# Kernel optimization log

Measured on AMD Instinct MI355X. Metric: run time of the kernel, lower is better.

The kernel has to match this reference:

```python
import jax, jax.numpy as jnp
import numpy as np

OT_REG = 0.1      # entropic regularization (ot_reg)
OT_TAU = 0.5      # marginal relaxation (ot_tau / reg_m)
N_ITERS = 100     # fixed Sinkhorn iterations (POT uses numItermax=1000 w/ stopThr=1e-6; 100 is converged here)


def setup_inputs() -> dict:
    key = jax.random.key(0)
    k1, k2 = jax.random.split(key)
    x = jax.random.normal(k1, (1, 4096, 1024), dtype=jnp.float32)
    y = jax.random.normal(k2, (1, 2048, 1024), dtype=jnp.float32)
    return {"x": x, "y": y}


def _sq_cdist(a, b):
    # torch.cdist(a, b) ** 2  ==  squared Euclidean pairwise distances, [N, M]
    d = (jnp.sum(a * a, axis=1)[:, None]
         + jnp.sum(b * b, axis=1)[None, :]
         - 2.0 * (a @ b.T))
    return jnp.maximum(d, 0.0)


def reference(x, y):
    # forward: squeeze leading batch dim, shift features to be >= 0 per row
    x = jnp.squeeze(x, axis=0)                      # [N, D]
    y = jnp.squeeze(y, axis=0)                      # [M, D]
    x = x - jnp.min(x, axis=-1, keepdims=True)
    y = y - jnp.min(y, axis=-1, keepdims=True)

    C = _sq_cdist(x, y)                              # [N, M] cost map (differentiable)
    n, m = C.shape

    # POT sinkhorn_knopp_unbalanced on detached, max-normalized cost
    Mn = jax.lax.stop_gradient(C)
    Mn = Mn / jnp.max(Mn)
    K = jnp.exp(-Mn / OT_REG)                        # Gibbs kernel
    a = jnp.full((n,), 1.0 / n, dtype=C.dtype)       # uniform source marginal
    b = jnp.full((m,), 1.0 / m, dtype=C.dtype)       # uniform target marginal
    fi = OT_TAU / (OT_TAU + OT_REG)

    def body(i, uv):
        u, v = uv
        u = (a / (K @ v)) ** fi
        v = (b / (K.T @ u)) ** fi
        return (u, v)

    u0 = jnp.full((n,), 1.0 / n, dtype=C.dtype)
    v0 = jnp.full((m,), 1.0 / m, dtype=C.dtype)
    u, v = jax.lax.fori_loop(0, N_ITERS, body, (u0, v0))

    flow = u[:, None] * K * v[None, :]               # [N, M] transport plan
    flow = jax.lax.stop_gradient(flow)               # plan is detached in original (numpy roundtrip)
    dist = jnp.sum(C * flow)                         # OT distance w/ grad through C only

    return flow.T[None], dist                        # pi.T.unsqueeze(0): [1, M, N]
```

## Files before the change

kernel.cpp:

```cpp
#include <hip/hip_runtime.h>


#define NROWS 4096
#define MCOLS 2048
#define NITER 100
#define NBLK  256
#define SPEC_TICKS 85ull

using short8  = __attribute__((ext_vector_type(8))) short;
using floatx4 = __attribute__((ext_vector_type(4))) float;

__device__ __forceinline__ float bf2f(unsigned short u) {
  return __uint_as_float(((unsigned)u) << 16);
}
__device__ __forceinline__ unsigned short f2bf(float f) {
  unsigned u = __float_as_uint(f);
  u += 0x7fffu + ((u >> 16) & 1u);
  return (unsigned short)(u >> 16);
}
__device__ __forceinline__ float powfi(float x, float fi) {
  return __expf(fi * __logf(x));
}
__device__ __forceinline__ unsigned packsp(float v, unsigned parity) {
  return __float_as_uint(v) | (parity << 31);
}
__device__ __forceinline__ unsigned aload(const unsigned* p) {
  return __hip_atomic_load(p, __ATOMIC_RELAXED, __HIP_MEMORY_SCOPE_AGENT);
}
__device__ __forceinline__ void astore(unsigned* p, unsigned v) {
  __hip_atomic_store(p, v, __ATOMIC_RELAXED, __HIP_MEMORY_SCOPE_AGENT);
}
__device__ __forceinline__ void gload_lds16(const unsigned short* gsrc, unsigned short* ldst) {
  __builtin_amdgcn_global_load_lds(
      (const __attribute__((address_space(1))) void*)gsrc,
      (__attribute__((address_space(3))) void*)ldst, 16, 0, 0);
}

__global__ __launch_bounds__(256) void prep_kernel(
    const float* __restrict__ x, const float* __restrict__ y,
    unsigned short* __restrict__ xb, unsigned short* __restrict__ yb,
    float* __restrict__ nx, float* __restrict__ ny,
    unsigned* __restrict__ maxCbits, float* __restrict__ out,
    unsigned* __restrict__ uglob, unsigned* __restrict__ vglob,
    unsigned* __restrict__ ublkflag, unsigned* __restrict__ vblkflag,
    unsigned* __restrict__ uroot, unsigned* __restrict__ vroot) {
  const int row = blockIdx.x;
  const int tid = threadIdx.x;

  if (row == 0) {
    if (tid == 0) { *maxCbits = 0u; out[8388608] = 0.0f; }
    #pragma unroll
    for (int k = 0; k < 16; ++k) uglob[tid + (k << 8)] = 0u;
    #pragma unroll
    for (int k = 0; k < 8; ++k) vglob[tid + (k << 8)] = 0u;
    ublkflag[tid] = 0u;
    vblkflag[tid] = 0u;
    if (tid < 32) { uroot[tid * 32] = 0u; vroot[tid * 32] = 0u; }
  }

  const float* src; unsigned short* dst; float* nd;
  if (row < NROWS) { src = x + (size_t)row * 1024; dst = xb + (size_t)row * 1024; nd = nx + row; }
  else { const int r = row - NROWS; src = y + (size_t)r * 1024; dst = yb + (size_t)r * 1024; nd = ny + r; }

  float4 v = ((const float4*)src)[tid];
  float mn = fminf(fminf(v.x, v.y), fminf(v.z, v.w));
  #pragma unroll
  for (int m = 1; m < 64; m <<= 1) mn = fminf(mn, __shfl_xor(mn, m));
  __shared__ float wred[4];
  const int w = tid >> 6, l = tid & 63;
  if (l == 0) wred[w] = mn;
  __syncthreads();
  mn = fminf(fminf(wred[0], wred[1]), fminf(wred[2], wred[3]));
  __syncthreads();

  const unsigned short b0 = f2bf(v.x - mn), b1 = f2bf(v.y - mn);
  const unsigned short b2 = f2bf(v.z - mn), b3 = f2bf(v.w - mn);
  ushort4 ub; ub.x = b0; ub.y = b1; ub.z = b2; ub.w = b3;
  ((ushort4*)dst)[tid] = ub;
  const float f0 = bf2f(b0), f1 = bf2f(b1), f2 = bf2f(b2), f3 = bf2f(b3);
  float acc = f0 * f0 + f1 * f1 + f2 * f2 + f3 * f3;
  #pragma unroll
  for (int m = 1; m < 64; m <<= 1) acc += __shfl_xor(acc, m);
  if (l == 0) wred[w] = acc;
  __syncthreads();
  if (tid == 0) *nd = wred[0] + wred[1] + wred[2] + wred[3];
}

__global__ __launch_bounds__(256) void cost_gemm_kernel(
    const unsigned short* __restrict__ xb, const unsigned short* __restrict__ yb,
    const float* __restrict__ nx, const float* __restrict__ ny,
    float* __restrict__ C, unsigned* __restrict__ maxCbits) {
  __shared__ __align__(16) unsigned short As[128 * 64];
  __shared__ __align__(16) unsigned short Bs[128 * 64];

  const int tid = threadIdx.x;
  const int w = tid >> 6, l = tid & 63;
  const int wr = w >> 1, wc = w & 1;
  const int i0 = blockIdx.y * 128;
  const int j0 = blockIdx.x * 128;
  const int m16 = l & 15, q = l >> 4;

  const int st_row = tid >> 3;
  const int st_s   = tid & 7;

  floatx4 acc[4][4];
  #pragma unroll
  for (int a = 0; a < 4; ++a)
    #pragma unroll
    for (int b = 0; b < 4; ++b) acc[a][b] = (floatx4){0.f, 0.f, 0.f, 0.f};

  for (int k0 = 0; k0 < 1024; k0 += 64) {
    #pragma unroll
    for (int c = 0; c < 4; ++c) {
      const int row = c * 32 + st_row;
      const int ss = st_s ^ (row & 7);
      gload_lds16(xb + (size_t)(i0 + row) * 1024 + k0 + ss * 8,
                  &As[c * 2048 + tid * 8]);
    }
    #pragma unroll
    for (int c = 0; c < 4; ++c) {
      const int row = c * 32 + st_row;
      const int ss = st_s ^ (row & 7);
      gload_lds16(yb + (size_t)(j0 + row) * 1024 + k0 + ss * 8,
                  &Bs[c * 2048 + tid * 8]);
    }
    __syncthreads();

    #pragma unroll
    for (int kk = 0; kk < 2; ++kk) {
      short8 av[4], bv[4];
      #pragma unroll
      for (int t = 0; t < 4; ++t) {
        const int row = wr * 64 + t * 16 + m16;
        const int slot = (kk * 4 + q) ^ (row & 7);
        av[t] = *(const short8*)&As[row * 64 + slot * 8];
      }
      #pragma unroll
      for (int t = 0; t < 4; ++t) {
        const int row = wc * 64 + t * 16 + m16;
        const int slot = (kk * 4 + q) ^ (row & 7);
        bv[t] = *(const short8*)&Bs[row * 64 + slot * 8];
      }
      #pragma unroll
      for (int ti = 0; ti < 4; ++ti)
        #pragma unroll
        for (int tj = 0; tj < 4; ++tj)
          acc[ti][tj] = __builtin_amdgcn_mfma_f32_16x16x32_bf16(av[ti], bv[tj], acc[ti][tj], 0, 0, 0);
    }
    __syncthreads();
  }

  float mx = 0.f;
  #pragma unroll
  for (int ti = 0; ti < 4; ++ti) {
    #pragma unroll
    for (int tj = 0; tj < 4; ++tj) {
      const int i = i0 + wr * 64 + ti * 16 + q * 4;
      const int j = j0 + wc * 64 + tj * 16 + m16;
      const float nyj = ny[j];
      #pragma unroll
      for (int r = 0; r < 4; ++r) {
        float c = nx[i + r] + nyj - 2.0f * acc[ti][tj][r];
        c = fmaxf(c, 0.0f);
        C[(size_t)(i + r) * 2048 + j] = c;
        mx = fmaxf(mx, c);
      }
    }
  }
  __shared__ float mred[4];
  #pragma unroll
  for (int m = 1; m < 64; m <<= 1) mx = fmaxf(mx, __shfl_xor(mx, m));
  if (l == 0) mred[w] = mx;
  __syncthreads();
  if (tid == 0) {
    const float bm = fmaxf(fmaxf(mred[0], mred[1]), fmaxf(mred[2], mred[3]));
    atomicMax(maxCbits, __float_as_uint(bm));
  }
}

__global__ __launch_bounds__(512) void sinkhorn_kernel(
    const float* __restrict__ C, const unsigned* __restrict__ maxCbits,
    unsigned* __restrict__ uglob, unsigned* __restrict__ vglob,
    unsigned* __restrict__ ublkflag, unsigned* __restrict__ vblkflag,
    unsigned* __restrict__ uroot, unsigned* __restrict__ vroot,
    float* __restrict__ out) {
  __shared__ __align__(16) unsigned short Ks[16 * 2048];
  __shared__ __align__(16) unsigned short KsT[8 * 4096];
  __shared__ __align__(16) float us[4096];
  __shared__ __align__(16) float vs[2048];
  __shared__ __align__(16) float uloc[16];
  __shared__ float dred[8];
  __shared__ unsigned needretry;

  const int tid = threadIdx.x;
  const int bid = blockIdx.x;
  const int w = tid >> 6, l = tid & 63;
  const int i0 = bid * 16;
  const int jb = bid * 8;

  const float fi = 0.8333333333333334f;
  const float av = 1.0f / 4096.0f;
  const float bv = 1.0f / 2048.0f;

  {
    if (tid == 0) needretry = 0u;
    const float sc = -1.0f / (0.1f * __uint_as_float(*maxCbits));
    for (int il = 0; il < 16; ++il) {
      const float* cp = C + (size_t)(i0 + il) * 2048 + tid * 4;
      const float4 c0 = *(const float4*)cp;
      uint2 pk;
      pk.x = (unsigned)f2bf(__expf(c0.x * sc)) | ((unsigned)f2bf(__expf(c0.y * sc)) << 16);
      pk.y = (unsigned)f2bf(__expf(c0.z * sc)) | ((unsigned)f2bf(__expf(c0.w * sc)) << 16);
      *(uint2*)&Ks[il * 2048 + tid * 4] = pk;
    }
    #pragma unroll
    for (int k = 0; k < 8; ++k) {
      const int i = tid + (k << 9);
      const float* cp = C + (size_t)i * 2048 + jb;
      const float4 c0 = *(const float4*)cp;
      const float4 c1 = *(const float4*)(cp + 4);
      KsT[0 * 4096 + i] = f2bf(__expf(c0.x * sc));
      KsT[1 * 4096 + i] = f2bf(__expf(c0.y * sc));
      KsT[2 * 4096 + i] = f2bf(__expf(c0.z * sc));
      KsT[3 * 4096 + i] = f2bf(__expf(c0.w * sc));
      KsT[4 * 4096 + i] = f2bf(__expf(c1.x * sc));
      KsT[5 * 4096 + i] = f2bf(__expf(c1.y * sc));
      KsT[6 * 4096 + i] = f2bf(__expf(c1.z * sc));
      KsT[7 * 4096 + i] = f2bf(__expf(c1.w * sc));
    }
    *(float4*)&vs[tid * 4] = make_float4(bv, bv, bv, bv);
  }
  __syncthreads();

  for (int it = 1; it <= NITER; ++it) {
    const unsigned tagit = (unsigned)it;
    const unsigned par = tagit & 1u;

    float part[2] = {0.f, 0.f};
    const int r0 = w * 2;
    #pragma unroll
    for (int c = 0; c < 4; ++c) {
      const int j0 = c * 512 + l * 8;
      const float4 va = *(const float4*)&vs[j0];
      const float4 vb = *(const float4*)&vs[j0 + 4];
      #pragma unroll
      for (int rr = 0; rr < 2; ++rr) {
        const uint4 kb = *(const uint4*)&Ks[(r0 + rr) * 2048 + j0];
        part[rr] += bf2f((unsigned short)kb.x) * va.x + bf2f((unsigned short)(kb.x >> 16)) * va.y
                 +  bf2f((unsigned short)kb.y) * va.z + bf2f((unsigned short)(kb.y >> 16)) * va.w
                 +  bf2f((unsigned short)kb.z) * vb.x + bf2f((unsigned short)(kb.z >> 16)) * vb.y
                 +  bf2f((unsigned short)kb.w) * vb.z + bf2f((unsigned short)(kb.w >> 16)) * vb.w;
      }
    }
    #pragma unroll
    for (int m = 1; m < 64; m <<= 1) {
      part[0] += __shfl_xor(part[0], m);
      part[1] += __shfl_xor(part[1], m);
    }
    if (l == 0) {
      #pragma unroll
      for (int r = 0; r < 2; ++r) {
        const float uv = powfi(av / part[r], fi);
        uloc[r0 + r] = uv;
        astore(&uglob[i0 + r0 + r], packsp(uv, par));
      }
    }
    __builtin_amdgcn_s_barrier();
    if (tid == 0) astore(&ublkflag[bid], tagit);
    const unsigned long long udl = __builtin_amdgcn_s_memrealtime() + SPEC_TICKS;

    if (bid == 0) {
      if (tid < 256)
        while ((int)(aload(&ublkflag[tid]) - tagit) < 0) __builtin_amdgcn_s_sleep(1);
      __builtin_amdgcn_s_barrier();
      if (tid < 32) astore(&uroot[tid * 32], tagit);
    }

    while (__builtin_amdgcn_s_memrealtime() < udl) __builtin_amdgcn_s_sleep(1);
    {
      unsigned pend = 0xFFu;
      unsigned gu[8];
      #pragma unroll
      for (int k = 0; k < 8; ++k)
        gu[k] = aload(&uglob[tid + (k << 9)]);
      #pragma unroll
      for (int k = 0; k < 8; ++k)
        if ((gu[k] >> 31) == par) {
          us[tid + (k << 9)] = __uint_as_float(gu[k] & 0x7FFFFFFFu);
          pend &= ~(1u << k);
        }
      if (pend) {
        #pragma unroll
        for (int k = 0; k < 8; ++k)
          if (pend & (1u << k))
            gu[k] = aload(&uglob[tid + (k << 9)]);
        #pragma unroll
        for (int k = 0; k < 8; ++k)
          if ((pend & (1u << k)) && (gu[k] >> 31) == par) {
            us[tid + (k << 9)] = __uint_as_float(gu[k] & 0x7FFFFFFFu);
            pend &= ~(1u << k);
          }
      }
      if (pend) atomicOr(&needretry, 1u);
      __syncthreads();
      if (needretry) {
        if (tid == 0)
          while ((int)(aload(&uroot[(bid & 31) * 32]) - tagit) < 0) __builtin_amdgcn_s_sleep(1);
        __syncthreads();
        while (pend) {
          #pragma unroll
          for (int k = 0; k < 8; ++k)
            if (pend & (1u << k))
              gu[k] = aload(&uglob[tid + (k << 9)]);
          #pragma unroll
          for (int k = 0; k < 8; ++k)
            if ((pend & (1u << k)) && (gu[k] >> 31) == par) {
              us[tid + (k << 9)] = __uint_as_float(gu[k] & 0x7FFFFFFFu);
              pend &= ~(1u << k);
            }
          if (pend) __builtin_amdgcn_s_sleep(1);
        }
        if (tid == 0) needretry = 0u;
        __syncthreads();
      }
    }

    {
      float t0 = 0.f;
      const int ca = w * 4096;
      #pragma unroll
      for (int c = 0; c < 8; ++c) {
        const int ic = c * 512 + l * 8;
        const float4 ua = *(const float4*)&us[ic];
        const float4 ub = *(const float4*)&us[ic + 4];
        const uint4 ka = *(const uint4*)&KsT[ca + ic];
        t0 += bf2f((unsigned short)ka.x) * ua.x + bf2f((unsigned short)(ka.x >> 16)) * ua.y
           +  bf2f((unsigned short)ka.y) * ua.z + bf2f((unsigned short)(ka.y >> 16)) * ua.w
           +  bf2f((unsigned short)ka.z) * ub.x + bf2f((unsigned short)(ka.z >> 16)) * ub.y
           +  bf2f((unsigned short)ka.w) * ub.z + bf2f((unsigned short)(ka.w >> 16)) * ub.w;
      }
      #pragma unroll
      for (int m = 1; m < 64; m <<= 1) t0 += __shfl_xor(t0, m);
      if (l == 0)
        astore(&vglob[jb + w], packsp(powfi(bv / t0, fi), par));
    }
    __builtin_amdgcn_s_barrier();
    if (tid == 0) astore(&vblkflag[bid], tagit);
    const unsigned long long vdl = __builtin_amdgcn_s_memrealtime() + SPEC_TICKS;

    if (bid == 1) {
      if (tid < 256)
        while ((int)(aload(&vblkflag[tid]) - tagit) < 0) __builtin_amdgcn_s_sleep(1);
      __builtin_amdgcn_s_barrier();
      if (tid < 32) astore(&vroot[tid * 32], tagit);
    }

    while (__builtin_amdgcn_s_memrealtime() < vdl) __builtin_amdgcn_s_sleep(1);
    {
      unsigned pend = 0xFu;
      unsigned gv[4];
      #pragma unroll
      for (int k = 0; k < 4; ++k)
        gv[k] = aload(&vglob[tid + (k << 9)]);
      #pragma unroll
      for (int k = 0; k < 4; ++k)
        if ((gv[k] >> 31) == par) {
          vs[tid + (k << 9)] = __uint_as_float(gv[k] & 0x7FFFFFFFu);
          pend &= ~(1u << k);
        }
      if (pend) {
        #pragma unroll
        for (int k = 0; k < 4; ++k)
          if (pend & (1u << k))
            gv[k] = aload(&vglob[tid + (k << 9)]);
        #pragma unroll
        for (int k = 0; k < 4; ++k)
          if ((pend & (1u << k)) && (gv[k] >> 31) == par) {
            vs[tid + (k << 9)] = __uint_as_float(gv[k] & 0x7FFFFFFFu);
            pend &= ~(1u << k);
          }
      }
      if (pend) atomicOr(&needretry, 1u);
      __syncthreads();
      if (needretry) {
        if (tid == 0)
          while ((int)(aload(&vroot[(bid & 31) * 32]) - tagit) < 0) __builtin_amdgcn_s_sleep(1);
        __syncthreads();
        while (pend) {
          #pragma unroll
          for (int k = 0; k < 4; ++k)
            if (pend & (1u << k))
              gv[k] = aload(&vglob[tid + (k << 9)]);
          #pragma unroll
          for (int k = 0; k < 4; ++k)
            if ((pend & (1u << k)) && (gv[k] >> 31) == par) {
              vs[tid + (k << 9)] = __uint_as_float(gv[k] & 0x7FFFFFFFu);
              pend &= ~(1u << k);
            }
          if (pend) __builtin_amdgcn_s_sleep(1);
        }
        if (tid == 0) needretry = 0u;
        __syncthreads();
      }
    }
  }

  float ur[16];
  *(float4*)&ur[0]  = *(const float4*)&uloc[0];
  *(float4*)&ur[4]  = *(const float4*)&uloc[4];
  *(float4*)&ur[8]  = *(const float4*)&uloc[8];
  *(float4*)&ur[12] = *(const float4*)&uloc[12];
  float distp = 0.f;
  for (int sub = 0; sub < 4; ++sub) {
    const int j = w * 256 + sub * 64 + l;
    const float vj = vs[j];
    float o[16];
    #pragma unroll
    for (int il = 0; il < 16; ++il) {
      const float kf = bf2f(Ks[il * 2048 + j]);
      const float fl = ur[il] * kf * vj;
      o[il] = fl;
      distp += C[(size_t)(i0 + il) * 2048 + j] * fl;
    }
    float* op = out + (size_t)j * 4096 + i0;
    *(float4*)(op)      = make_float4(o[0],  o[1],  o[2],  o[3]);
    *(float4*)(op + 4)  = make_float4(o[4],  o[5],  o[6],  o[7]);
    *(float4*)(op + 8)  = make_float4(o[8],  o[9],  o[10], o[11]);
    *(float4*)(op + 12) = make_float4(o[12], o[13], o[14], o[15]);
  }
  #pragma unroll
  for (int m = 1; m < 64; m <<= 1) distp += __shfl_xor(distp, m);
  if (l == 0) dred[w] = distp;
  __syncthreads();
  if (tid == 0) {
    float ds = 0.f;
    #pragma unroll
    for (int k = 0; k < 8; ++k) ds += dred[k];
    unsafeAtomicAdd(out + (size_t)8388608, ds);
  }
}

extern "C" void kernel_launch(void* const* d_in, const int* in_sizes, int n_in,
                              void* d_out, int out_size, void* d_ws, size_t ws_size,
                              hipStream_t stream) {
  (void)in_sizes; (void)n_in; (void)out_size; (void)ws_size;
  const float* x = (const float*)d_in[0];
  const float* y = (const float*)d_in[1];
  float* out = (float*)d_out;
  char* ws = (char*)d_ws;

  float*              Cmat     = (float*)(ws + 0);
  unsigned short*     xb       = (unsigned short*)(ws + 33554432);
  unsigned short*     yb       = (unsigned short*)(ws + 41943040);
  float*              nx       = (float*)(ws + 46137344);
  float*              ny       = (float*)(ws + 46153728);
  unsigned*           maxC     = (unsigned*)(ws + 46161920);
  unsigned*           uglob    = (unsigned*)(ws + 46162432);
  unsigned*           vglob    = (unsigned*)(ws + 46178816);
  unsigned*           ublkflag = (unsigned*)(ws + 46187008);
  unsigned*           vblkflag = (unsigned*)(ws + 46188032);
  unsigned*           uroot    = (unsigned*)(ws + 46189056);
  unsigned*           vroot    = (unsigned*)(ws + 46193152);

  hipLaunchKernelGGL(prep_kernel, dim3(6144), dim3(256), 0, stream, x, y, xb, yb, nx, ny,
                     maxC, out, uglob, vglob, ublkflag, vblkflag, uroot, vroot);
  hipLaunchKernelGGL(cost_gemm_kernel, dim3(16, 32), dim3(256), 0, stream, xb, yb, nx, ny, Cmat, maxC);
  hipLaunchKernelGGL(sinkhorn_kernel, dim3(NBLK), dim3(512), 0, stream,
                     Cmat, maxC, uglob, vglob, ublkflag, vblkflag, uroot, vroot, out);
}
```

Baseline: 638.5 us.

## Double Sinkhorn block size to 1024 threads, one row per wave

Launches the persistent Sinkhorn kernel with 1024 threads per block instead of 512. Each of the 16 waves now handles one u-row, and pairs of waves split each v-column dot product, combined through shared memory. The gather, setup and epilogue loops are re-indexed for the larger block. The goal is to shorten the per-iteration critical path by spreading the matvec work over more waves. The cost is an extra __syncthreads and shared reduction in the v step, plus higher register pressure under the 1024-thread launch bound.

```diff
diff --git a/kernel.cpp b/kernel.cpp
--- a/kernel.cpp
+++ b/kernel.cpp
@@ -178,7 +178,7 @@
   }
 }
 
-__global__ __launch_bounds__(512) void sinkhorn_kernel(
+__global__ __launch_bounds__(1024) void sinkhorn_kernel(
     const float* __restrict__ C, const unsigned* __restrict__ maxCbits,
     unsigned* __restrict__ uglob, unsigned* __restrict__ vglob,
     unsigned* __restrict__ ublkflag, unsigned* __restrict__ vblkflag,
@@ -189,7 +189,8 @@
   __shared__ __align__(16) float us[4096];
   __shared__ __align__(16) float vs[2048];
   __shared__ __align__(16) float uloc[16];
-  __shared__ float dred[8];
+  __shared__ float wred16[16];
+  __shared__ float dred[16];
   __shared__ unsigned needretry;
 
   const int tid = threadIdx.x;
@@ -206,16 +207,15 @@
     if (tid == 0) needretry = 0u;
     const float sc = -1.0f / (0.1f * __uint_as_float(*maxCbits));
     for (int il = 0; il < 16; ++il) {
-      const float* cp = C + (size_t)(i0 + il) * 2048 + tid * 4;
-      const float4 c0 = *(const float4*)cp;
-      uint2 pk;
-      pk.x = (unsigned)f2bf(__expf(c0.x * sc)) | ((unsigned)f2bf(__expf(c0.y * sc)) << 16);
-      pk.y = (unsigned)f2bf(__expf(c0.z * sc)) | ((unsigned)f2bf(__expf(c0.w * sc)) << 16);
-      *(uint2*)&Ks[il * 2048 + tid * 4] = pk;
-    }
-    #pragma unroll
-    for (int k = 0; k < 8; ++k) {
-      const int i = tid + (k << 9);
+      const float* cp = C + (size_t)(i0 + il) * 2048 + tid * 2;
+      const float2 c0 = *(const float2*)cp;
+      const unsigned pk = (unsigned)f2bf(__expf(c0.x * sc))
+                        | ((unsigned)f2bf(__expf(c0.y * sc)) << 16);
+      *(unsigned*)&Ks[il * 2048 + tid * 2] = pk;
+    }
+    #pragma unroll
+    for (int k = 0; k < 4; ++k) {
+      const int i = tid + (k << 10);
       const float* cp = C + (size_t)i * 2048 + jb;
       const float4 c0 = *(const float4*)cp;
       const float4 c1 = *(const float4*)(cp + 4);
@@ -228,7 +228,7 @@
       KsT[6 * 4096 + i] = f2bf(__expf(c1.z * sc));
       KsT[7 * 4096 + i] = f2bf(__expf(c1.w * sc));
     }
-    *(float4*)&vs[tid * 4] = make_float4(bv, bv, bv, bv);
+    *(float2*)&vs[tid * 2] = make_float2(bv, bv);
   }
   __syncthreads();
 
@@ -236,34 +236,24 @@
     const unsigned tagit = (unsigned)it;
     const unsigned par = tagit & 1u;
 
-    float part[2] = {0.f, 0.f};
-    const int r0 = w * 2;
+    float part = 0.f;
     #pragma unroll
     for (int c = 0; c < 4; ++c) {
       const int j0 = c * 512 + l * 8;
       const float4 va = *(const float4*)&vs[j0];
       const float4 vb = *(const float4*)&vs[j0 + 4];
-      #pragma unroll
-      for (int rr = 0; rr < 2; ++rr) {
-        const uint4 kb = *(const uint4*)&Ks[(r0 + rr) * 2048 + j0];
-        part[rr] += bf2f((unsigned short)kb.x) * va.x + bf2f((unsigned short)(kb.x >> 16)) * va.y
-                 +  bf2f((unsigned short)kb.y) * va.z + bf2f((unsigned short)(kb.y >> 16)) * va.w
-                 +  bf2f((unsigned short)kb.z) * vb.x + bf2f((unsigned short)(kb.z >> 16)) * vb.y
-                 +  bf2f((unsigned short)kb.w) * vb.z + bf2f((unsigned short)(kb.w >> 16)) * vb.w;
-      }
-    }
-    #pragma unroll
-    for (int m = 1; m < 64; m <<= 1) {
-      part[0] += __shfl_xor(part[0], m);
-      part[1] += __shfl_xor(part[1], m);
-    }
+      const uint4 kb = *(const uint4*)&Ks[w * 2048 + j0];
+      part += bf2f((unsigned short)kb.x) * va.x + bf2f((unsigned short)(kb.x >> 16)) * va.y
+           +  bf2f((unsigned short)kb.y) * va.z + bf2f((unsigned short)(kb.y >> 16)) * va.w
+           +  bf2f((unsigned short)kb.z) * vb.x + bf2f((unsigned short)(kb.z >> 16)) * vb.y
+           +  bf2f((unsigned short)kb.w) * vb.z + bf2f((unsigned short)(kb.w >> 16)) * vb.w;
+    }
+    #pragma unroll
+    for (int m = 1; m < 64; m <<= 1) part += __shfl_xor(part, m);
     if (l == 0) {
-      #pragma unroll
-      for (int r = 0; r < 2; ++r) {
-        const float uv = powfi(av / part[r], fi);
-        uloc[r0 + r] = uv;
-        astore(&uglob[i0 + r0 + r], packsp(uv, par));
-      }
+      const float uv = powfi(av / part, fi);
+      uloc[w] = uv;
+      astore(&uglob[i0 + w], packsp(uv, par));
     }
     __builtin_amdgcn_s_barrier();
     if (tid == 0) astore(&ublkflag[bid], tagit);
@@ -278,26 +268,26 @@
 
     while (__builtin_amdgcn_s_memrealtime() < udl) __builtin_amdgcn_s_sleep(1);
     {
-      unsigned pend = 0xFFu;
-      unsigned gu[8];
-      #pragma unroll
-      for (int k = 0; k < 8; ++k)
-        gu[k] = aload(&uglob[tid + (k << 9)]);
-      #pragma unroll
-      for (int k = 0; k < 8; ++k)
+      unsigned pend = 0xFu;
+      unsigned gu[4];
+      #pragma unroll
+      for (int k = 0; k < 4; ++k)
+        gu[k] = aload(&uglob[tid + (k << 10)]);
+      #pragma unroll
+      for (int k = 0; k < 4; ++k)
         if ((gu[k] >> 31) == par) {
-          us[tid + (k << 9)] = __uint_as_float(gu[k] & 0x7FFFFFFFu);
+          us[tid + (k << 10)] = __uint_as_float(gu[k] & 0x7FFFFFFFu);
           pend &= ~(1u << k);
         }
       if (pend) {
         #pragma unroll
-        for (int k = 0; k < 8; ++k)
+        for (int k = 0; k < 4; ++k)
           if (pend & (1u << k))
-            gu[k] = aload(&uglob[tid + (k << 9)]);
+            gu[k] = aload(&uglob[tid + (k << 10)]);
         #pragma unroll
-        for (int k = 0; k < 8; ++k)
+        for (int k = 0; k < 4; ++k)
           if ((pend & (1u << k)) && (gu[k] >> 31) == par) {
-            us[tid + (k << 9)] = __uint_as_float(gu[k] & 0x7FFFFFFFu);
+            us[tid + (k << 10)] = __uint_as_float(gu[k] & 0x7FFFFFFFu);
             pend &= ~(1u << k);
           }
       }
@@ -309,13 +299,13 @@
         __syncthreads();
         while (pend) {
           #pragma unroll
-          for (int k = 0; k < 8; ++k)
+          for (int k = 0; k < 4; ++k)
             if (pend & (1u << k))
-              gu[k] = aload(&uglob[tid + (k << 9)]);
+              gu[k] = aload(&uglob[tid + (k << 10)]);
           #pragma unroll
-          for (int k = 0; k < 8; ++k)
+          for (int k = 0; k < 4; ++k)
             if ((pend & (1u << k)) && (gu[k] >> 31) == par) {
-              us[tid + (k << 9)] = __uint_as_float(gu[k] & 0x7FFFFFFFu);
+              us[tid + (k << 10)] = __uint_as_float(gu[k] & 0x7FFFFFFFu);
               pend &= ~(1u << k);
             }
           if (pend) __builtin_amdgcn_s_sleep(1);
@@ -327,10 +317,11 @@
 
     {
       float t0 = 0.f;
-      const int ca = w * 4096;
-      #pragma unroll
-      for (int c = 0; c < 8; ++c) {
-        const int ic = c * 512 + l * 8;
+      const int col = w >> 1, h = w & 1;
+      const int ca = col * 4096;
+      #pragma unroll
+      for (int c = 0; c < 4; ++c) {
+        const int ic = h * 2048 + c * 512 + l * 8;
         const float4 ua = *(const float4*)&us[ic];
         const float4 ub = *(const float4*)&us[ic + 4];
         const uint4 ka = *(const uint4*)&KsT[ca + ic];
@@ -341,8 +332,12 @@
       }
       #pragma unroll
       for (int m = 1; m < 64; m <<= 1) t0 += __shfl_xor(t0, m);
-      if (l == 0)
-        astore(&vglob[jb + w], packsp(powfi(bv / t0, fi), par));
+      if (l == 0) wred16[w] = t0;
+    }
+    __syncthreads();
+    if (tid < 8) {
+      const float tot = wred16[2 * tid] + wred16[2 * tid + 1];
+      astore(&vglob[jb + tid], packsp(powfi(bv / tot, fi), par));
     }
     __builtin_amdgcn_s_barrier();
     if (tid == 0) astore(&vblkflag[bid], tagit);
@@ -357,26 +352,26 @@
 
     while (__builtin_amdgcn_s_memrealtime() < vdl) __builtin_amdgcn_s_sleep(1);
     {
-      unsigned pend = 0xFu;
-      unsigned gv[4];
-      #pragma unroll
-      for (int k = 0; k < 4; ++k)
-        gv[k] = aload(&vglob[tid + (k << 9)]);
-      #pragma unroll
-      for (int k = 0; k < 4; ++k)
+      unsigned pend = 0x3u;
+      unsigned gv[2];
+      #pragma unroll
+      for (int k = 0; k < 2; ++k)
+        gv[k] = aload(&vglob[tid + (k << 10)]);
+      #pragma unroll
+      for (int k = 0; k < 2; ++k)
         if ((gv[k] >> 31) == par) {
-          vs[tid + (k << 9)] = __uint_as_float(gv[k] & 0x7FFFFFFFu);
+          vs[tid + (k << 10)] = __uint_as_float(gv[k] & 0x7FFFFFFFu);
           pend &= ~(1u << k);
         }
       if (pend) {
         #pragma unroll
-        for (int k = 0; k < 4; ++k)
+        for (int k = 0; k < 2; ++k)
           if (pend & (1u << k))
-            gv[k] = aload(&vglob[tid + (k << 9)]);
+            gv[k] = aload(&vglob[tid + (k << 10)]);
         #pragma unroll
-        for (int k = 0; k < 4; ++k)
+        for (int k = 0; k < 2; ++k)
           if ((pend & (1u << k)) && (gv[k] >> 31) == par) {
-            vs[tid + (k << 9)] = __uint_as_float(gv[k] & 0x7FFFFFFFu);
+            vs[tid + (k << 10)] = __uint_as_float(gv[k] & 0x7FFFFFFFu);
             pend &= ~(1u << k);
           }
       }
@@ -388,13 +383,13 @@
         __syncthreads();
         while (pend) {
           #pragma unroll
-          for (int k = 0; k < 4; ++k)
+          for (int k = 0; k < 2; ++k)
             if (pend & (1u << k))
-              gv[k] = aload(&vglob[tid + (k << 9)]);
+              gv[k] = aload(&vglob[tid + (k << 10)]);
           #pragma unroll
-          for (int k = 0; k < 4; ++k)
+          for (int k = 0; k < 2; ++k)
             if ((pend & (1u << k)) && (gv[k] >> 31) == par) {
-              vs[tid + (k << 9)] = __uint_as_float(gv[k] & 0x7FFFFFFFu);
+              vs[tid + (k << 10)] = __uint_as_float(gv[k] & 0x7FFFFFFFu);
               pend &= ~(1u << k);
             }
           if (pend) __builtin_amdgcn_s_sleep(1);
@@ -411,8 +406,8 @@
   *(float4*)&ur[8]  = *(const float4*)&uloc[8];
   *(float4*)&ur[12] = *(const float4*)&uloc[12];
   float distp = 0.f;
-  for (int sub = 0; sub < 4; ++sub) {
-    const int j = w * 256 + sub * 64 + l;
+  for (int sub = 0; sub < 2; ++sub) {
+    const int j = w * 128 + sub * 64 + l;
     const float vj = vs[j];
     float o[16];
     #pragma unroll
@@ -435,7 +430,7 @@
   if (tid == 0) {
     float ds = 0.f;
     #pragma unroll
-    for (int k = 0; k < 8; ++k) ds += dred[k];
+    for (int k = 0; k < 16; ++k) ds += dred[k];
     unsafeAtomicAdd(out + (size_t)8388608, ds);
   }
 }
@@ -465,6 +460,6 @@
   hipLaunchKernelGGL(prep_kernel, dim3(6144), dim3(256), 0, stream, x, y, xb, yb, nx, ny,
                      maxC, out, uglob, vglob, ublkflag, vblkflag, uroot, vroot);
   hipLaunchKernelGGL(cost_gemm_kernel, dim3(16, 32), dim3(256), 0, stream, xb, yb, nx, ny, Cmat, maxC);
-  hipLaunchKernelGGL(sinkhorn_kernel, dim3(NBLK), dim3(512), 0, stream,
+  hipLaunchKernelGGL(sinkhorn_kernel, dim3(NBLK), dim3(1024), 0, stream,
                      Cmat, maxC, uglob, vglob, ublkflag, vblkflag, uroot, vroot, out);
 }
```

Result: no change. 650.3 us (+1.9%).
